# Kernel tuning notes

Measured on AMD Instinct MI355X. Metric: run time of the kernel, lower is better.

The kernel has to match this reference:

```python
import jax, jax.numpy as jnp
import numpy as np

NUM_HEADS = 4
NEG_INF = -1e9  # finite large-negative to avoid inf*weight -> nan in head combiner


def setup_inputs() -> dict:
    key = jax.random.key(0)
    k1, k2, k3, k4, k5 = jax.random.split(key, 5)
    B, S, T = 16, 1024, 512
    Q, E = 256, 512
    src_encodings = jax.random.normal(k1, (B, S, E), dtype=jnp.float32)
    src_token_mask = jax.random.randint(k2, (B, S), 0, 2).astype(jnp.bool_)
    query_vec = jax.random.normal(k3, (T, B, Q), dtype=jnp.float32)
    # Linear(src_encoding_size, query_vec_size * numheads, bias=False)
    W_src = jax.random.normal(k4, (E, Q * NUM_HEADS), dtype=jnp.float32) * (1.0 / np.sqrt(E))
    # Linear(numheads, 1, bias=False) -> combiner vector of shape (numheads,)
    w_comb = jax.random.normal(k5, (NUM_HEADS,), dtype=jnp.float32) * 0.5
    return {"src_encodings": src_encodings, "src_token_mask": src_token_mask,
            "query_vec": query_vec, "W_src": W_src, "w_comb": w_comb}


def reference(src_encodings, src_token_mask, query_vec, W_src, w_comb):
    # project + leaky_relu: (B,S,E) @ (E,H*Q) -> (B,S,H*Q)
    proj = jax.nn.leaky_relu(src_encodings @ W_src)
    B, S, _ = proj.shape
    Q = query_vec.shape[-1]
    proj = proj.reshape(B, S, NUM_HEADS, Q)                 # (B,S,H,Q)
    # per-head attention scores against each query step: (T,B,S,H)
    scores = jnp.einsum('bshq,tbq->tbsh', proj, query_vec)
    # mask invalid source tokens along S (broadcast over T and heads)
    scores = jnp.where(src_token_mask[None, :, :, None], NEG_INF, scores)
    # multihead combiner Linear(H,1,bias=False): (T,B,S)
    weights = jnp.einsum('tbsh,h->tbs', scores, w_comb)
    return jax.nn.softmax(weights, axis=-1)
```

## Files before the change

### kernel.cpp

```cpp
#include <hip/hip_runtime.h>
#include <hip/hip_bf16.h>
#include <cstdint>

constexpr int Bn = 16;
constexpr int Sn = 1024;
constexpr int Tn = 512;
constexpr int QD = 256;
constexpr int En = 512;
constexpr int Hn = 4;
constexpr float SLOPE = 0.01f;
constexpr float NEG_INF = -1e9f;
constexpr int Mn = Bn * Sn;

typedef _Float16 f16;
typedef f16 f16x4 __attribute__((ext_vector_type(4)));
typedef f16 f16x8 __attribute__((ext_vector_type(8)));
typedef float f32x4 __attribute__((ext_vector_type(4)));

#define G2L(g, l) __builtin_amdgcn_global_load_lds(                      \
    (const __attribute__((address_space(1))) void*)(g),                  \
    (__attribute__((address_space(3))) void*)(l), 16, 0, 0)

#define VM6 asm volatile("s_waitcnt vmcnt(6)" ::: "memory")
#define VM4 asm volatile("s_waitcnt vmcnt(4)" ::: "memory")
#define VM0 asm volatile("s_waitcnt vmcnt(0)" ::: "memory")
#define LG0 asm volatile("s_waitcnt lgkmcnt(0)" ::: "memory")

__global__ __launch_bounds__(256) void prep_kernel(
    const float* __restrict__ src, const float* __restrict__ W,
    const unsigned char* __restrict__ mask_bytes,
    f16* __restrict__ Ah, f16* __restrict__ Al,
    f16* __restrict__ Bht, f16* __restrict__ Blt,
    int* __restrict__ flag)
{
    __shared__ float T[64][65];
    __shared__ int cnt;
    const int bid = blockIdx.x;
    const int tid = threadIdx.x;

    if (bid < 8192) {
        const size_t i4 = (size_t)bid * 256 + tid;
        const size_t base = i4 * 4;
        const float4 v = *(const float4*)(src + base);
        f16x4 hi, lo;
        const float xs[4] = {v.x, v.y, v.z, v.w};
        #pragma unroll
        for (int j = 0; j < 4; ++j) {
            f16 h = (f16)xs[j];
            hi[j] = h;
            lo[j] = (f16)(xs[j] - (float)h);
        }
        *(f16x4*)(Ah + base) = hi;
        *(f16x4*)(Al + base) = lo;
    } else if (bid < 8320) {
        const int nb = bid - 8192;
        const int n0 = (nb & 15) * 64;
        const int k0 = (nb >> 4) * 64;
        #pragma unroll
        for (int p = 0; p < 4; ++p) {
            const int e = p * 256 + tid;
            const int r = e >> 4;
            const int c4 = e & 15;
            const float4 v = *(const float4*)(W + (size_t)(k0 + r) * (Hn * QD) + n0 + c4 * 4);
            T[r][c4 * 4 + 0] = v.x; T[r][c4 * 4 + 1] = v.y;
            T[r][c4 * 4 + 2] = v.z; T[r][c4 * 4 + 3] = v.w;
        }
        __syncthreads();
        #pragma unroll
        for (int p = 0; p < 4; ++p) {
            const int e = p * 256 + tid;
            const int r = e >> 4;
            const int c4 = e & 15;
            f16x4 hi, lo;
            #pragma unroll
            for (int j = 0; j < 4; ++j) {
                const float x = T[c4 * 4 + j][r];
                f16 h = (f16)x;
                hi[j] = h;
                lo[j] = (f16)(x - (float)h);
            }
            const size_t off = (size_t)(n0 + r) * En + k0 + c4 * 4;
            *(f16x4*)(Bht + off) = hi;
            *(f16x4*)(Blt + off) = lo;
        }
    } else {
        if (tid == 0) cnt = 0;
        __syncthreads();
        int local = 0;
        for (int p = tid; p < 4096; p += 256) {
            if ((p & 3) != 0 && mask_bytes[p] != 0) local++;
        }
        atomicAdd(&cnt, local);
        __syncthreads();
        if (tid == 0) flag[0] = (cnt == 0) ? 1 : 0;
    }
}

__global__ __launch_bounds__(256) void conv_q_kernel(
    const float* __restrict__ query, f16* __restrict__ Qh, f16* __restrict__ Ql)
{
    const int tid = threadIdx.x;
    const int rloc = tid >> 6;
    const int lane = tid & 63;
    const int row = blockIdx.x * 4 + rloc;
    const int t = row >> 4, b = row & 15;
    const float4 v = *(const float4*)(query + (size_t)row * QD + lane * 4);
    f16x4 hi, lo;
    const float xs[4] = {v.x, v.y, v.z, v.w};
    #pragma unroll
    for (int j = 0; j < 4; ++j) {
        f16 h = (f16)xs[j];
        hi[j] = h;
        lo[j] = (f16)(xs[j] - (float)h);
    }
    const size_t off = ((size_t)(b * Tn + t)) * QD + lane * 4;
    *(f16x4*)(Qh + off) = hi;
    *(f16x4*)(Ql + off) = lo;
}

__global__ __launch_bounds__(256) void gemm1_kernel(
    const f16* __restrict__ Ah, const f16* __restrict__ Al,
    const f16* __restrict__ Bht, const f16* __restrict__ Blt,
    const float* __restrict__ wcomb,
    f16* __restrict__ Ch, f16* __restrict__ Cl)
{
    __shared__ f16 lds_f[36864];

    const int tid = threadIdx.x;
    const int l  = tid & 63;
    const int wv = tid >> 6;
    const int wm = wv >> 1;
    const int wn = wv & 1;

    const int bid = blockIdx.x;
    const int swz = (bid & 7) * 64 + (bid >> 3);
    const int m0 = (swz >> 2) * 128;
    const int q0 = (swz & 3) * 64;

    const int rc  = tid >> 2;
    const int xk  = ((tid & 3) ^ ((tid >> 3) & 3)) * 8;
    const int stgA = (m0 + rc) * En + xk;
    const int stgB = (q0 + rc) * En + xk;

    const int xf  = (l >> 1) & 3;
    const int kx  = ((l >> 4) ^ xf) * 8;
    const int aFrag = (wm * 64 + (l & 15)) * 32 + kx;
    const int bFrag = 4096 + (wn * 32 + (l & 15)) * 32 + kx;

    f32x4 acc[4][8];
    #pragma unroll
    for (int m = 0; m < 4; ++m)
        #pragma unroll
        for (int f = 0; f < 8; ++f) acc[m][f] = (f32x4){0.f, 0.f, 0.f, 0.f};

    auto stage1 = [&](int t) {
        const f16* As = (t < 16) ? Ah : ((t < 32) ? Al : Ah);
        const f16* Bs = (t < 32) ? Bht : Blt;
        const int kofs = (t & 15) * 32;
        f16* dst = lds_f + (t % 3) * 12288 + wv * 512;
        G2L(As + stgA + kofs,                dst);
        G2L(As + stgA + 64 * En + kofs,      dst + 2048);
        G2L(Bs + stgB + kofs,                dst + 4096);
        G2L(Bs + stgB + QD * En + kofs,      dst + 4096 + 2048);
        G2L(Bs + stgB + 2 * QD * En + kofs,  dst + 4096 + 4096);
        G2L(Bs + stgB + 3 * QD * En + kofs,  dst + 4096 + 6144);
    };

    stage1(0);
    stage1(1);
    VM6;
    __builtin_amdgcn_s_barrier();

    #pragma unroll
    for (int t = 0; t < 48; ++t) {
        if (t + 2 < 48) stage1(t + 2);
        const f16* Lb = lds_f + (t % 3) * 12288;
        f16x8 af[4], bfr[8];
        #pragma unroll
        for (int m = 0; m < 4; ++m) af[m] = *(const f16x8*)(Lb + aFrag + m * 512);
        #pragma unroll
        for (int f = 0; f < 8; ++f)
            bfr[f] = *(const f16x8*)(Lb + bFrag + (f >> 1) * 2048 + (f & 1) * 512);
        __builtin_amdgcn_s_setprio(1);
        #pragma unroll
        for (int m = 0; m < 4; ++m) {
            #pragma unroll
            for (int f = 0; f < 8; ++f)
                acc[m][f] = __builtin_amdgcn_mfma_f32_16x16x32_f16(
                    af[m], bfr[f], acc[m][f], 0, 0, 0);
        }
        __builtin_amdgcn_s_setprio(0);
        if (t <= 45)      VM6;
        else if (t == 46) VM0;
        LG0;
        __builtin_amdgcn_s_barrier();
    }

    const float w0 = wcomb[0], w1 = wcomb[1], w2 = wcomb[2], w3 = wcomb[3];
    const int rbase = m0 + wm * 64 + (l >> 4) * 4;
    #pragma unroll
    for (int m = 0; m < 4; ++m) {
        #pragma unroll
        for (int qs = 0; qs < 2; ++qs) {
            const int q = q0 + wn * 32 + qs * 16 + (l & 15);
            #pragma unroll
            for (int i = 0; i < 4; ++i) {
                float x0 = acc[m][0 + qs][i]; x0 = x0 >= 0.f ? x0 : SLOPE * x0;
                float x1 = acc[m][2 + qs][i]; x1 = x1 >= 0.f ? x1 : SLOPE * x1;
                float x2 = acc[m][4 + qs][i]; x2 = x2 >= 0.f ? x2 : SLOPE * x2;
                float x3 = acc[m][6 + qs][i]; x3 = x3 >= 0.f ? x3 : SLOPE * x3;
                const float c = w0 * x0 + w1 * x1 + w2 * x2 + w3 * x3;
                const f16 ch = (f16)c;
                const f16 cl = (f16)(c - (float)ch);
                const size_t off = (size_t)(rbase + m * 16 + i) * QD + q;
                Ch[off] = ch;
                Cl[off] = cl;
            }
        }
    }
}

__global__ __launch_bounds__(256) void gemm2_kernel(
    const f16* __restrict__ Ch, const f16* __restrict__ Cl,
    const f16* __restrict__ Qh, const f16* __restrict__ Ql,
    const void* __restrict__ maskp, const float* __restrict__ wcomb,
    const int* __restrict__ flag,
    float* __restrict__ out)
{
    __shared__ f16 lds2[24576];

    const int tid = threadIdx.x;
    const int l  = tid & 63;
    const int wv = tid >> 6;
    const int wm = wv >> 1;
    const int wn = wv & 1;

    const int bid = blockIdx.x;
    const int swz = (bid & 7) * 64 + (bid >> 3);
    const int b   = swz >> 5;
    const int s0  = ((swz >> 2) & 7) * 128;
    const int t0  = (swz & 3) * 128;

    const int rowc = tid >> 2;
    const int xk   = ((tid & 3) ^ ((rowc >> 1) & 3)) * 8;
    const int stgA = (b * Sn + s0 + rowc) * QD + xk;
    const int stgB = (b * Tn + t0 + rowc) * QD + xk;

    const int xf  = ((l >> 1) & 3);
    const int aFrag = (wm * 64 + (l & 15)) * 32 + (((l >> 4) ^ xf) * 8);
    const int bFrag = 4096 + (wn * 64 + (l & 15)) * 32 + (((l >> 4) ^ xf) * 8);

    f32x4 acc[4][4];
    #pragma unroll
    for (int m = 0; m < 4; ++m)
        #pragma unroll
        for (int n = 0; n < 4; ++n) acc[m][n] = (f32x4){0.f, 0.f, 0.f, 0.f};

    auto stage1 = [&](int t) {
        const f16* As = (t < 8) ? Ch : ((t < 16) ? Cl : Ch);
        const f16* Bs = (t < 16) ? Qh : Ql;
        const int kofs = (t & 7) * 32;
        f16* dst = lds2 + (t % 3) * 8192 + wv * 512;
        G2L(As + stgA + kofs,           dst);
        G2L(As + stgA + 64 * QD + kofs, dst + 2048);
        G2L(Bs + stgB + kofs,           dst + 4096);
        G2L(Bs + stgB + 64 * QD + kofs, dst + 4096 + 2048);
    };

    stage1(0);
    stage1(1);
    VM4;
    __builtin_amdgcn_s_barrier();

    #pragma unroll
    for (int kt = 0; kt < 24; ++kt) {
        if (kt + 2 < 24) stage1(kt + 2);
        const f16* Lb = lds2 + (kt % 3) * 8192;
        f16x8 af[4], bfr[4];
        #pragma unroll
        for (int m = 0; m < 4; ++m) af[m] = *(const f16x8*)(Lb + aFrag + m * 512);
        #pragma unroll
        for (int n = 0; n < 4; ++n) bfr[n] = *(const f16x8*)(Lb + bFrag + n * 512);
        __builtin_amdgcn_s_setprio(1);
        #pragma unroll
        for (int m = 0; m < 4; ++m) {
            #pragma unroll
            for (int n = 0; n < 4; ++n)
                acc[m][n] = __builtin_amdgcn_mfma_f32_16x16x32_f16(
                    af[m], bfr[n], acc[m][n], 0, 0, 0);
        }
        __builtin_amdgcn_s_setprio(0);
        if (kt <= 21)      VM4;
        else if (kt == 22) VM0;
        LG0;
        __builtin_amdgcn_s_barrier();
    }

    const float sumw = wcomb[0] + wcomb[1] + wcomb[2] + wcomb[3];
    const float maskval = NEG_INF * sumw;
    const bool is_int = (flag[0] != 0);
    const int rbase = s0 + wm * 64 + (l >> 4) * 4;

    bool msk[4][4];
    #pragma unroll
    for (int m = 0; m < 4; ++m)
        #pragma unroll
        for (int i = 0; i < 4; ++i) {
            const int idx = b * Sn + rbase + m * 16 + i;
            int mm;
            if (is_int) mm = ((const int*)maskp)[idx];
            else        mm = (int)((const unsigned char*)maskp)[idx];
            msk[m][i] = (mm != 0);
        }

    #pragma unroll
    for (int m = 0; m < 4; ++m)
        #pragma unroll
        for (int n = 0; n < 4; ++n) {
            const int t = t0 + wn * 64 + n * 16 + (l & 15);
            float vals[4];
            #pragma unroll
            for (int i = 0; i < 4; ++i)
                vals[i] = msk[m][i] ? maskval : acc[m][n][i];
            *(float4*)(out + ((size_t)t * Bn + b) * Sn + rbase + m * 16)
                = make_float4(vals[0], vals[1], vals[2], vals[3]);
        }
}

__global__ __launch_bounds__(256) void softmax_kernel(float* __restrict__ out) {
    const int bid = blockIdx.x;
    const int k = bid & 7;
    const int r = bid >> 3;
    const int b = (k << 1) | (r & 1);
    const int t = r >> 1;
    const size_t row = (size_t)t * Bn + b;
    float* p = out + row * (size_t)Sn;
    const int tid = threadIdx.x;
    const int lane = tid & 63, wave = tid >> 6;

    float4 v = ((const float4*)p)[tid];

    float m = fmaxf(fmaxf(v.x, v.y), fmaxf(v.z, v.w));
    #pragma unroll
    for (int off = 32; off; off >>= 1) m = fmaxf(m, __shfl_down(m, off));
    __shared__ float smax[4];
    __shared__ float sm_all;
    if (lane == 0) smax[wave] = m;
    __syncthreads();
    if (tid == 0) sm_all = fmaxf(fmaxf(smax[0], smax[1]), fmaxf(smax[2], smax[3]));
    __syncthreads();
    m = sm_all;

    float e0 = __expf(v.x - m), e1 = __expf(v.y - m);
    float e2 = __expf(v.z - m), e3 = __expf(v.w - m);
    float s = e0 + e1 + e2 + e3;
    #pragma unroll
    for (int off = 32; off; off >>= 1) s += __shfl_down(s, off);
    __shared__ float ssum[4];
    __shared__ float ss_all;
    if (lane == 0) ssum[wave] = s;
    __syncthreads();
    if (tid == 0) ss_all = ssum[0] + ssum[1] + ssum[2] + ssum[3];
    __syncthreads();
    const float inv = 1.0f / ss_all;

    ((float4*)p)[tid] = make_float4(e0 * inv, e1 * inv, e2 * inv, e3 * inv);
}

extern "C" void kernel_launch(void* const* d_in, const int* in_sizes, int n_in,
                              void* d_out, int out_size, void* d_ws, size_t ws_size,
                              hipStream_t stream) {
    const float* src   = (const float*)d_in[0];
    const void*  maskp = d_in[1];
    const float* query = (const float*)d_in[2];
    const float* Wsrc  = (const float*)d_in[3];
    const float* wcomb = (const float*)d_in[4];
    float* out = (float*)d_out;

    constexpr size_t MB = 1024 * 1024;
    char* ws = (char*)d_ws;
    int* flag = (int*)ws;
    f16* Ah  = (f16*)(ws + 256);
    f16* Al  = (f16*)(ws + 256 + 16 * MB);
    f16* Bht = (f16*)(ws + 256 + 32 * MB);
    f16* Blt = (f16*)(ws + 256 + 33 * MB);
    f16* Ch  = (f16*)(ws + 256 + 34 * MB);
    f16* Cl  = (f16*)(ws + 256 + 42 * MB);
    f16* Qh  = (f16*)(ws + 256);
    f16* Ql  = (f16*)(ws + 256 + 4 * MB);

    prep_kernel<<<8321, 256, 0, stream>>>(
        src, Wsrc, (const unsigned char*)maskp, Ah, Al, Bht, Blt, flag);

    gemm1_kernel<<<512, 256, 0, stream>>>(Ah, Al, Bht, Blt, wcomb, Ch, Cl);

    conv_q_kernel<<<(Tn * Bn) / 4, 256, 0, stream>>>(query, Qh, Ql);

    gemm2_kernel<<<512, 256, 0, stream>>>(Ch, Cl, Qh, Ql, maskp, wcomb, flag, out);

    softmax_kernel<<<Tn * Bn, 256, 0, stream>>>(out);
}
```

Before: 115.2 us.

## Fuse fp32-to-fp16 split of src into gemm1 A loads and merge query conversion into prep

gemm1 now reads src directly as fp32 through registers, splits each value into hi/lo fp16 on the fly and writes it into LDS. This removes the separate pass that wrote the 32MB Ah/Al workspace and the gemm1 reads of it. The query conversion moves into prep_kernel, so there is one fewer launch. In exchange the A operand no longer uses async global-to-LDS loads, which adds register pressure and an extra convert-and-store step inside the pipelined loop. src is also re-read once per K pass (three passes in total).

```diff
diff --git a/kernel.cpp b/kernel.cpp
--- a/kernel.cpp
+++ b/kernel.cpp
@@ -21,16 +21,15 @@
     (const __attribute__((address_space(1))) void*)(g),                  \
     (__attribute__((address_space(3))) void*)(l), 16, 0, 0)
 
-#define VM6 asm volatile("s_waitcnt vmcnt(6)" ::: "memory")
 #define VM4 asm volatile("s_waitcnt vmcnt(4)" ::: "memory")
 #define VM0 asm volatile("s_waitcnt vmcnt(0)" ::: "memory")
 #define LG0 asm volatile("s_waitcnt lgkmcnt(0)" ::: "memory")
 
 __global__ __launch_bounds__(256) void prep_kernel(
-    const float* __restrict__ src, const float* __restrict__ W,
+    const float* __restrict__ W, const float* __restrict__ query,
     const unsigned char* __restrict__ mask_bytes,
-    f16* __restrict__ Ah, f16* __restrict__ Al,
     f16* __restrict__ Bht, f16* __restrict__ Blt,
+    f16* __restrict__ Qh, f16* __restrict__ Ql,
     int* __restrict__ flag)
 {
     __shared__ float T[64][65];
@@ -38,24 +37,9 @@
     const int bid = blockIdx.x;
     const int tid = threadIdx.x;
 
-    if (bid < 8192) {
-        const size_t i4 = (size_t)bid * 256 + tid;
-        const size_t base = i4 * 4;
-        const float4 v = *(const float4*)(src + base);
-        f16x4 hi, lo;
-        const float xs[4] = {v.x, v.y, v.z, v.w};
-        #pragma unroll
-        for (int j = 0; j < 4; ++j) {
-            f16 h = (f16)xs[j];
-            hi[j] = h;
-            lo[j] = (f16)(xs[j] - (float)h);
-        }
-        *(f16x4*)(Ah + base) = hi;
-        *(f16x4*)(Al + base) = lo;
-    } else if (bid < 8320) {
-        const int nb = bid - 8192;
-        const int n0 = (nb & 15) * 64;
-        const int k0 = (nb >> 4) * 64;
+    if (bid < 128) {
+        const int n0 = (bid & 15) * 64;
+        const int k0 = (bid >> 4) * 64;
         #pragma unroll
         for (int p = 0; p < 4; ++p) {
             const int e = p * 256 + tid;
@@ -83,6 +67,23 @@
             *(f16x4*)(Bht + off) = hi;
             *(f16x4*)(Blt + off) = lo;
         }
+    } else if (bid < 2176) {
+        const int rloc = tid >> 6;
+        const int lane = tid & 63;
+        const int row = (bid - 128) * 4 + rloc;
+        const int t = row >> 4, b = row & 15;
+        const float4 v = *(const float4*)(query + (size_t)row * QD + lane * 4);
+        f16x4 hi, lo;
+        const float xs[4] = {v.x, v.y, v.z, v.w};
+        #pragma unroll
+        for (int j = 0; j < 4; ++j) {
+            f16 h = (f16)xs[j];
+            hi[j] = h;
+            lo[j] = (f16)(xs[j] - (float)h);
+        }
+        const size_t off = ((size_t)(b * Tn + t)) * QD + lane * 4;
+        *(f16x4*)(Qh + off) = hi;
+        *(f16x4*)(Ql + off) = lo;
     } else {
         if (tid == 0) cnt = 0;
         __syncthreads();
@@ -96,30 +97,8 @@
     }
 }
 
-__global__ __launch_bounds__(256) void conv_q_kernel(
-    const float* __restrict__ query, f16* __restrict__ Qh, f16* __restrict__ Ql)
-{
-    const int tid = threadIdx.x;
-    const int rloc = tid >> 6;
-    const int lane = tid & 63;
-    const int row = blockIdx.x * 4 + rloc;
-    const int t = row >> 4, b = row & 15;
-    const float4 v = *(const float4*)(query + (size_t)row * QD + lane * 4);
-    f16x4 hi, lo;
-    const float xs[4] = {v.x, v.y, v.z, v.w};
-    #pragma unroll
-    for (int j = 0; j < 4; ++j) {
-        f16 h = (f16)xs[j];
-        hi[j] = h;
-        lo[j] = (f16)(xs[j] - (float)h);
-    }
-    const size_t off = ((size_t)(b * Tn + t)) * QD + lane * 4;
-    *(f16x4*)(Qh + off) = hi;
-    *(f16x4*)(Ql + off) = lo;
-}
-
 __global__ __launch_bounds__(256) void gemm1_kernel(
-    const f16* __restrict__ Ah, const f16* __restrict__ Al,
+    const float* __restrict__ src,
     const f16* __restrict__ Bht, const f16* __restrict__ Blt,
     const float* __restrict__ wcomb,
     f16* __restrict__ Ch, f16* __restrict__ Cl)
@@ -138,9 +117,13 @@
     const int q0 = (swz & 3) * 64;
 
     const int rc  = tid >> 2;
-    const int xk  = ((tid & 3) ^ ((tid >> 3) & 3)) * 8;
-    const int stgA = (m0 + rc) * En + xk;
-    const int stgB = (q0 + rc) * En + xk;
+    const int xkB = ((tid & 3) ^ ((tid >> 3) & 3)) * 8;
+    const int stgB = (q0 + rc) * En + xkB;
+
+    const int arow0 = tid >> 3;
+    const int ak8   = tid & 7;
+    const int axr   = (arow0 >> 1) & 3;
+    const int aslot = arow0 * 32 + (((ak8 >> 1) ^ axr) * 8) + (ak8 & 1) * 4;
 
     const int xf  = (l >> 1) & 3;
     const int kx  = ((l >> 4) ^ xf) * 8;
@@ -153,27 +136,51 @@
         #pragma unroll
         for (int f = 0; f < 8; ++f) acc[m][f] = (f32x4){0.f, 0.f, 0.f, 0.f};
 
-    auto stage1 = [&](int t) {
-        const f16* As = (t < 16) ? Ah : ((t < 32) ? Al : Ah);
+    float4 a4[4];
+    auto issueA = [&](int t) {
+        const int k0 = (t & 15) * 32;
+        #pragma unroll
+        for (int j = 0; j < 4; ++j)
+            a4[j] = *(const float4*)(src + (size_t)(m0 + arow0 + j * 32) * En
+                                     + k0 + ak8 * 4);
+    };
+    auto writeA = [&](int t) {
+        const bool lo = (t >= 16) && (t < 32);
+        f16* slotA = lds_f + (t % 3) * 12288;
+        #pragma unroll
+        for (int j = 0; j < 4; ++j) {
+            const float xs[4] = {a4[j].x, a4[j].y, a4[j].z, a4[j].w};
+            f16x4 hv;
+            #pragma unroll
+            for (int e = 0; e < 4; ++e) {
+                f16 h = (f16)xs[e];
+                hv[e] = lo ? (f16)(xs[e] - (float)h) : h;
+            }
+            *(f16x4*)(slotA + j * 1024 + aslot) = hv;
+        }
+    };
+    auto stageB1 = [&](int t) {
         const f16* Bs = (t < 32) ? Bht : Blt;
         const int kofs = (t & 15) * 32;
-        f16* dst = lds_f + (t % 3) * 12288 + wv * 512;
-        G2L(As + stgA + kofs,                dst);
-        G2L(As + stgA + 64 * En + kofs,      dst + 2048);
-        G2L(Bs + stgB + kofs,                dst + 4096);
-        G2L(Bs + stgB + QD * En + kofs,      dst + 4096 + 2048);
-        G2L(Bs + stgB + 2 * QD * En + kofs,  dst + 4096 + 4096);
-        G2L(Bs + stgB + 3 * QD * En + kofs,  dst + 4096 + 6144);
+        f16* dst = lds_f + (t % 3) * 12288 + 4096 + wv * 512;
+        G2L(Bs + stgB + kofs,                dst);
+        G2L(Bs + stgB + QD * En + kofs,      dst + 2048);
+        G2L(Bs + stgB + 2 * QD * En + kofs,  dst + 4096);
+        G2L(Bs + stgB + 3 * QD * En + kofs,  dst + 6144);
     };
 
-    stage1(0);
-    stage1(1);
-    VM6;
+    issueA(0);
+    stageB1(0);
+    stageB1(1);
+    VM4;
+    writeA(0);
+    LG0;
     __builtin_amdgcn_s_barrier();
 
     #pragma unroll
     for (int t = 0; t < 48; ++t) {
-        if (t + 2 < 48) stage1(t + 2);
+        if (t + 1 < 48) issueA(t + 1);
+        if (t + 2 < 48) stageB1(t + 2);
         const f16* Lb = lds_f + (t % 3) * 12288;
         f16x8 af[4], bfr[8];
         #pragma unroll
@@ -190,8 +197,9 @@
                     af[m], bfr[f], acc[m][f], 0, 0, 0);
         }
         __builtin_amdgcn_s_setprio(0);
-        if (t <= 45)      VM6;
+        if (t <= 45)      VM4;
         else if (t == 46) VM0;
+        if (t + 1 < 48) writeA(t + 1);
         LG0;
         __builtin_amdgcn_s_barrier();
     }
@@ -380,21 +388,17 @@
     constexpr size_t MB = 1024 * 1024;
     char* ws = (char*)d_ws;
     int* flag = (int*)ws;
-    f16* Ah  = (f16*)(ws + 256);
-    f16* Al  = (f16*)(ws + 256 + 16 * MB);
-    f16* Bht = (f16*)(ws + 256 + 32 * MB);
-    f16* Blt = (f16*)(ws + 256 + 33 * MB);
-    f16* Ch  = (f16*)(ws + 256 + 34 * MB);
-    f16* Cl  = (f16*)(ws + 256 + 42 * MB);
     f16* Qh  = (f16*)(ws + 256);
     f16* Ql  = (f16*)(ws + 256 + 4 * MB);
-
-    prep_kernel<<<8321, 256, 0, stream>>>(
-        src, Wsrc, (const unsigned char*)maskp, Ah, Al, Bht, Blt, flag);
-
-    gemm1_kernel<<<512, 256, 0, stream>>>(Ah, Al, Bht, Blt, wcomb, Ch, Cl);
-
-    conv_q_kernel<<<(Tn * Bn) / 4, 256, 0, stream>>>(query, Qh, Ql);
+    f16* Bht = (f16*)(ws + 256 + 8 * MB);
+    f16* Blt = (f16*)(ws + 256 + 9 * MB);
+    f16* Ch  = (f16*)(ws + 256 + 10 * MB);
+    f16* Cl  = (f16*)(ws + 256 + 18 * MB);
+
+    prep_kernel<<<2177, 256, 0, stream>>>(
+        Wsrc, query, (const unsigned char*)maskp, Bht, Blt, Qh, Ql, flag);
+
+    gemm1_kernel<<<512, 256, 0, stream>>>(src, Bht, Blt, wcomb, Ch, Cl);
 
     gemm2_kernel<<<512, 256, 0, stream>>>(Ch, Cl, Qh, Ql, maskp, wcomb, flag, out);
 
```

After: 118.4 us. +2.7%, slower.
